# Optimization experiments

Hardware: AMD Instinct MI355X
Metric: run time of the kernel (lower is better)

The kernel has to match this reference:

```python
import jax, jax.numpy as jnp
import numpy as np

N = 16384   # total nodes
M = 512     # molecules
D_IN = 64
D_OUT = 64
NEG = -1e9  # mask value for nodes outside a molecule


def setup_inputs() -> dict:
    key = jax.random.key(0)
    ks = jax.random.split(key, 8)
    node_features = jax.random.normal(ks[0], (N, D_IN), dtype=jnp.float32)
    e = jax.random.uniform(ks[1], (N, N), dtype=jnp.float32) * (2.0 / N)
    # molecule membership: sorted segment ids -> one-hot membership matrix
    seg = np.sort(np.asarray(jax.random.randint(ks[2], (N,), 0, M)))
    mnm = (seg[None, :] == np.arange(M)[:, None]).astype(np.float32)
    mol_node_matrix = jnp.asarray(mnm)
    mol_node_mask = jnp.asarray((1.0 - mnm) * NEG)
    s = 1.0 / np.sqrt(D_IN)
    W0 = jax.random.uniform(ks[3], (D_OUT, D_IN), jnp.float32, -s, s)
    b0 = jnp.zeros((D_OUT,), jnp.float32)
    W1 = jax.random.uniform(ks[4], (D_OUT, D_OUT), jnp.float32, -s, s)
    b1 = jnp.zeros((D_OUT,), jnp.float32)
    w2 = jax.random.uniform(ks[5], (1, D_OUT), jnp.float32, -s, s)
    b2 = jnp.zeros((1,), jnp.float32)
    return dict(node_features=node_features, e=e,
                mol_node_matrix=mol_node_matrix, mol_node_mask=mol_node_mask,
                W0=W0, b0=b0, W1=W1, b1=b1, w2=w2, b2=b2)


def reference(node_features, e, mol_node_matrix, mol_node_mask, W0, b0, W1, b1, w2, b2):
    # GraphConvolutionLayer: two linears with adjacency matmul, LeakyReLU between
    h = e @ (node_features @ W0.T + b0)            # [N, D_OUT]
    h = jax.nn.leaky_relu(h, negative_slope=0.01)
    h = e @ (h @ W1.T + b1)                        # [N, D_OUT]
    h = jnp.tanh(h)
    # attention logits per node; mol_node_matrix @ diag(a) == mnm * a^T (broadcast)
    a = (h @ w2.T + b2).reshape(-1)                # [N]
    logits = mol_node_matrix * a[None, :] + mol_node_mask  # [M, N]
    mol_node_weight = jax.nn.softmax(logits, axis=1)
    return mol_node_weight @ h, mol_node_weight
```

## Files before the change

kernel.cpp:

```cpp
#include <hip/hip_runtime.h>
#include <hip/hip_bf16.h>

#define NN 16384
#define MM 512
#define DD 64
#define BK 128
#define BM 32
#define ITERS (NN / BK)
#define BK2 256
#define ITERS2 (NN / BK2)

typedef __attribute__((ext_vector_type(8))) short short8;
typedef __attribute__((ext_vector_type(4))) float f32x4;
typedef __attribute__((ext_vector_type(4))) short short4v;
typedef __attribute__((ext_vector_type(4))) unsigned u32x4;

#define SE 2097152.0f
#define INV_SE 4.76837158203125e-07f

__device__ __forceinline__ short f2bf(float f) {
  union { __hip_bfloat16 b; short s; } u;
  u.b = __float2bfloat16(f);
  return u.s;
}

__device__ __forceinline__ short8 cvt8(f32x4 a, f32x4 b) {
  short8 r;
  r[0] = f2bf(a[0]); r[1] = f2bf(a[1]); r[2] = f2bf(a[2]); r[3] = f2bf(a[3]);
  r[4] = f2bf(b[0]); r[5] = f2bf(b[1]); r[6] = f2bf(b[2]); r[7] = f2bf(b[3]);
  return r;
}

typedef __attribute__((address_space(1))) const unsigned gu32;
typedef __attribute__((address_space(3))) unsigned lu32;
__device__ __forceinline__ void gld16(const void* g, void* l) {
  __builtin_amdgcn_global_load_lds((gu32*)g, (lu32*)l, 16, 0, 0);
}

template <int OFMT>
__global__ __launch_bounds__(256) void linear_mfma(const float* __restrict__ in,
                                                   const float* __restrict__ W,
                                                   const float* __restrict__ b,
                                                   void* __restrict__ xt_) {
  const int t = threadIdx.x, lane = t & 63, w = t >> 6;
  const int rl = lane & 15, hi = lane >> 4;
  const int r0 = blockIdx.x * 64 + w * 16;
  const float* ap = in + (size_t)(r0 + rl) * DD + hi * 8;

  f32x4 acc[4];
#pragma unroll
  for (int g = 0; g < 4; ++g) {
    const float bias = b[g * 16 + rl];
    acc[g][0] = bias; acc[g][1] = bias; acc[g][2] = bias; acc[g][3] = bias;
  }
#pragma unroll
  for (int kk = 0; kk < DD; kk += 32) {
    const short8 af = cvt8(*(const f32x4*)(ap + kk), *(const f32x4*)(ap + kk + 4));
#pragma unroll
    for (int g = 0; g < 4; ++g) {
      const float* wp = W + (size_t)(g * 16 + rl) * DD + hi * 8 + kk;
      const short8 wf = cvt8(*(const f32x4*)wp, *(const f32x4*)(wp + 4));
      acc[g] = __builtin_amdgcn_mfma_f32_16x16x32_bf16(af, wf, acc[g], 0, 0, 0);
    }
  }
#pragma unroll
  for (int g = 0; g < 4; ++g) {
    if (OFMT == 0) {
      unsigned short* xt = (unsigned short*)xt_;
      short4v s;
      s[0] = f2bf(acc[g][0]); s[1] = f2bf(acc[g][1]);
      s[2] = f2bf(acc[g][2]); s[3] = f2bf(acc[g][3]);
      *(short4v*)(xt + (size_t)(g * 16 + rl) * NN + r0 + hi * 4) = s;
    } else {
      unsigned char* xt = (unsigned char*)xt_;
      int pk = __builtin_amdgcn_cvt_pk_fp8_f32(acc[g][0], acc[g][1], 0, false);
      pk = __builtin_amdgcn_cvt_pk_fp8_f32(acc[g][2], acc[g][3], pk, true);
      *(unsigned*)(xt + (size_t)(g * 16 + rl) * NN + r0 + hi * 4) = (unsigned)pk;
    }
  }
}

__global__ __launch_bounds__(256) void gemm1(const float* __restrict__ e,
                                             const unsigned short* __restrict__ xt,
                                             float* __restrict__ out,
                                             unsigned char* __restrict__ e8) {
  __shared__ float Ab[2][BM * BK];
  __shared__ unsigned short Bb[2][64 * BK];
  const int t = threadIdx.x, lane = t & 63, w = t >> 6;
  const int rl = lane & 15, hi = lane >> 4;
  const int wr = w >> 1, wc = w & 1;
  const int r0 = blockIdx.x * BM;
  const int it0 = (blockIdx.x * 37) & (ITERS - 1);

  auto STAGE = [&](int buf, int it) {
    const int k0 = ((it0 + it) & (ITERS - 1)) * BK;
#pragma unroll
    for (int j = 0; j < 4; ++j) {
      const int row = w * 8 + j * 2 + (lane >> 5);
      const float* src =
          e + (size_t)(r0 + row) * NN + k0 + (((lane & 31) ^ (row & 7)) << 2);
      gld16(src, &Ab[buf][(w * 8 + j * 2) * BK]);
    }
#pragma unroll
    for (int j = 0; j < 4; ++j) {
      const int col = w * 16 + j * 4 + (lane >> 4);
      const unsigned short* src =
          xt + (size_t)col * NN + k0 + (((lane & 15) ^ (col & 7)) << 3);
      gld16(src, &Bb[buf][(w * 16 + j * 4) * BK]);
    }
  };

  f32x4 acc[2];
  acc[0][0] = acc[0][1] = acc[0][2] = acc[0][3] = 0.f;
  acc[1][0] = acc[1][1] = acc[1][2] = acc[1][3] = 0.f;

  STAGE(0, 0);
#pragma unroll 1
  for (int it = 0; it < ITERS; ++it) {
    const int cur = it & 1;
    const int k0c = ((it0 + it) & (ITERS - 1)) * BK;
    if (it + 1 < ITERS) {
      STAGE(cur ^ 1, it + 1);
      asm volatile("s_waitcnt vmcnt(9)" ::: "memory");
    } else {
      asm volatile("s_waitcnt vmcnt(0)" ::: "memory");
    }
    __builtin_amdgcn_s_barrier();
    asm volatile("" ::: "memory");
#pragma unroll
    for (int kk = 0; kk < BK; kk += 32) {
      const int ca = (kk >> 2) + hi * 2;
      const int arow = (wr * 16 + rl) * BK;
      f32x4 a0 = *(const f32x4*)&Ab[cur][arow + ((ca ^ (rl & 7)) << 2)];
      f32x4 a1 = *(const f32x4*)&Ab[cur][arow + (((ca + 1) ^ (rl & 7)) << 2)];
      const short8 af = cvt8(a0, a1);
      const int cb = (kk >> 3) + hi;
#pragma unroll
      for (int g = 0; g < 2; ++g) {
        const int col = wc * 32 + g * 16 + rl;
        const short8 bf =
            *(const short8*)&Bb[cur][col * BK + ((cb ^ (rl & 7)) << 3)];
        acc[g] = __builtin_amdgcn_mfma_f32_16x16x32_bf16(af, bf, acc[g], 0, 0, 0);
      }
    }
    {
      const int r = t >> 3, j0 = t & 7;
      const float* arow = &Ab[cur][r * BK];
      u32x4 dw;
#pragma unroll
      for (int i = 0; i < 4; ++i) {
        const int c = j0 * 4 + i;
        f32x4 q = *(const f32x4*)&arow[(c ^ (r & 7)) << 2];
        int d = __builtin_amdgcn_cvt_pk_fp8_f32(q[0] * SE, q[1] * SE, 0, false);
        d = __builtin_amdgcn_cvt_pk_fp8_f32(q[2] * SE, q[3] * SE, d, true);
        dw[i] = (unsigned)d;
      }
      *(u32x4*)(e8 + (size_t)(r0 + r) * NN + k0c + j0 * 16) = dw;
    }
    asm volatile("" ::: "memory");
    __builtin_amdgcn_s_barrier();
  }

#pragma unroll
  for (int g = 0; g < 2; ++g) {
    const int col = wc * 32 + g * 16 + rl;
#pragma unroll
    for (int j = 0; j < 4; ++j) {
      float v = acc[g][j];
      v = (v > 0.f) ? v : 0.01f * v;
      out[(size_t)(r0 + wr * 16 + hi * 4 + j) * DD + col] = v;
    }
  }
}

__global__ __launch_bounds__(256) void gemm2_fp8(const unsigned char* __restrict__ e8,
                                                 const unsigned char* __restrict__ xt8,
                                                 float* __restrict__ out) {
  __shared__ unsigned char Ab2[2][BM * BK2];
  __shared__ unsigned char Bb2[2][64 * BK2];
  const int t = threadIdx.x, lane = t & 63, w = t >> 6;
  const int rl = lane & 15, hi = lane >> 4;
  const int wr = w >> 1, wc = w & 1;
  const int r0 = blockIdx.x * BM;
  const int it0 = (blockIdx.x * 37) & (ITERS2 - 1);

  auto STAGE = [&](int buf, int it) {
    const int k0 = ((it0 + it) & (ITERS2 - 1)) * BK2;
#pragma unroll
    for (int j = 0; j < 2; ++j) {
      const int row = w * 8 + j * 4 + (lane >> 4);
      const unsigned char* src =
          e8 + (size_t)(r0 + row) * NN + k0 + (((lane & 15) ^ (row & 15)) << 4);
      gld16(src, &Ab2[buf][(w * 8 + j * 4) * BK2]);
    }
#pragma unroll
    for (int j = 0; j < 4; ++j) {
      const int col = w * 16 + j * 4 + (lane >> 4);
      const unsigned char* src =
          xt8 + (size_t)col * NN + k0 + (((lane & 15) ^ (col & 15)) << 4);
      gld16(src, &Bb2[buf][(w * 16 + j * 4) * BK2]);
    }
  };

  f32x4 acc[2];
  acc[0][0] = acc[0][1] = acc[0][2] = acc[0][3] = 0.f;
  acc[1][0] = acc[1][1] = acc[1][2] = acc[1][3] = 0.f;

  STAGE(0, 0);
#pragma unroll 1
  for (int it = 0; it < ITERS2; ++it) {
    const int cur = it & 1;
    if (it + 1 < ITERS2) {
      STAGE(cur ^ 1, it + 1);
      asm volatile("s_waitcnt vmcnt(6)" ::: "memory");
    } else {
      asm volatile("s_waitcnt vmcnt(0)" ::: "memory");
    }
    __builtin_amdgcn_s_barrier();
    asm volatile("" ::: "memory");
    const unsigned char* arow = &Ab2[cur][(wr * 16 + rl) * BK2];
#pragma unroll
    for (int kk = 0; kk < BK2; kk += 32) {
      const int ca = (kk >> 4) + (hi >> 1);
      const int off = (hi & 1) * 8;
      const long af = *(const long*)&arow[((ca ^ (rl & 15)) << 4) + off];
#pragma unroll
      for (int g = 0; g < 2; ++g) {
        const int col = wc * 32 + g * 16 + rl;
        const long bf =
            *(const long*)&Bb2[cur][col * BK2 + ((ca ^ (col & 15)) << 4) + off];
        acc[g] = __builtin_amdgcn_mfma_f32_16x16x32_fp8_fp8(af, bf, acc[g], 0, 0, 0);
      }
    }
    asm volatile("" ::: "memory");
    __builtin_amdgcn_s_barrier();
  }

#pragma unroll
  for (int g = 0; g < 2; ++g) {
    const int col = wc * 32 + g * 16 + rl;
#pragma unroll
    for (int j = 0; j < 4; ++j) {
      float v = tanhf(acc[g][j] * INV_SE);
      out[(size_t)(r0 + wr * 16 + hi * 4 + j) * DD + col] = v;
    }
  }
}

__global__ __launch_bounds__(256) void a_kernel(const float* __restrict__ h,
                                                const float* __restrict__ w2,
                                                const float* __restrict__ b2,
                                                float* __restrict__ a) {
  const int t = threadIdx.x;
  const int lane = t & 63;
  const int n = blockIdx.x * 4 + (t >> 6);
  float v = h[(size_t)n * DD + lane] * w2[lane];
#pragma unroll
  for (int off = 32; off > 0; off >>= 1) v += __shfl_xor(v, off);
  if (lane == 0) a[n] = v + b2[0];
}

__global__ __launch_bounds__(256) void softmax_kernel(const float* __restrict__ mnm,
                                                      const float* __restrict__ a,
                                                      float* __restrict__ wout) {
  __shared__ float red[256];
  const int m = blockIdx.x, t = threadIdx.x;
  const size_t base = (size_t)m * NN;
  const f32x4* mnm4 = (const f32x4*)(mnm + base);
  const f32x4* a4 = (const f32x4*)a;
  f32x4* wout4 = (f32x4*)(wout + base);

  f32x4 lg[16];
  float mx = -3.0e38f;
#pragma unroll
  for (int i = 0; i < 16; ++i) {
    const int idx = t + i * 256;
    const f32x4 mv = mnm4[idx];
    const f32x4 av = a4[idx];
    f32x4 v;
#pragma unroll
    for (int j = 0; j < 4; ++j) v[j] = (mv[j] > 0.5f) ? av[j] : -3.0e38f;
    lg[i] = v;
    mx = fmaxf(mx, fmaxf(fmaxf(v[0], v[1]), fmaxf(v[2], v[3])));
  }
  red[t] = mx; __syncthreads();
  for (int s = 128; s > 0; s >>= 1) {
    if (t < s) red[t] = fmaxf(red[t], red[t + s]);
    __syncthreads();
  }
  mx = red[0]; __syncthreads();
  const bool empty = (mx < -1.0e38f);
  float sm = 0.f;
#pragma unroll
  for (int i = 0; i < 16; ++i) {
    f32x4 v = lg[i];
#pragma unroll
    for (int j = 0; j < 4; ++j)
      v[j] = empty ? 1.0f : ((v[j] > -1.0e38f) ? expf(v[j] - mx) : 0.0f);
    lg[i] = v;
    sm += v[0] + v[1] + v[2] + v[3];
  }
  red[t] = sm; __syncthreads();
  for (int s = 128; s > 0; s >>= 1) {
    if (t < s) red[t] += red[t + s];
    __syncthreads();
  }
  const float inv = 1.0f / red[0];
#pragma unroll
  for (int i = 0; i < 16; ++i) wout4[t + i * 256] = lg[i] * inv;
}

__global__ __launch_bounds__(256) void pool_kernel(const float* __restrict__ wmat,
                                                   const float* __restrict__ h,
                                                   float* __restrict__ out0) {
  __shared__ float wl[256];
  __shared__ float partial[4][64];
  const int m = blockIdx.x;
  const int t = threadIdx.x;
  const int d = t & 63;
  const int sub = t >> 6;
  float acc = 0.f;
  for (int c0 = 0; c0 < NN; c0 += 256) {
    float wv = wmat[(size_t)m * NN + c0 + t];
    __syncthreads();
    wl[t] = wv;
    if (__syncthreads_or(wv > 0.f)) {
      const float* hp = h + (size_t)(c0 + sub * 64) * DD + d;
      const float* wp = wl + sub * 64;
#pragma unroll 8
      for (int i = 0; i < 64; ++i) acc += wp[i] * hp[(size_t)i * DD];
    }
  }
  __syncthreads();
  partial[sub][d] = acc;
  __syncthreads();
  if (t < 64)
    out0[m * DD + t] =
        partial[0][t] + partial[1][t] + partial[2][t] + partial[3][t];
}

extern "C" void kernel_launch(void* const* d_in, const int* in_sizes, int n_in,
                              void* d_out, int out_size, void* d_ws, size_t ws_size,
                              hipStream_t stream) {
  const float* nf  = (const float*)d_in[0];
  const float* e   = (const float*)d_in[1];
  const float* mnm = (const float*)d_in[2];
  const float* W0  = (const float*)d_in[4];
  const float* b0  = (const float*)d_in[5];
  const float* W1  = (const float*)d_in[6];
  const float* b1  = (const float*)d_in[7];
  const float* w2  = (const float*)d_in[8];
  const float* b2  = (const float*)d_in[9];

  char* ws = (char*)d_ws;
  unsigned short* XT0 = (unsigned short*)(ws);
  unsigned char*  XT8 = (unsigned char*)(ws + (size_t)2 * 1024 * 1024);
  float* h1 = (float*)(ws + (size_t)4 * 1024 * 1024);
  float* h  = (float*)(ws + (size_t)8 * 1024 * 1024);
  float* av = (float*)(ws + (size_t)12 * 1024 * 1024);
  unsigned char* e8 = (unsigned char*)(ws + (size_t)16 * 1024 * 1024);

  float* out0 = (float*)d_out;
  float* wout = out0 + (size_t)MM * DD;

  linear_mfma<0><<<256, 256, 0, stream>>>(nf, W0, b0, XT0);
  gemm1<<<512, 256, 0, stream>>>(e, XT0, h1, e8);
  linear_mfma<1><<<256, 256, 0, stream>>>(h1, W1, b1, XT8);
  gemm2_fp8<<<512, 256, 0, stream>>>(e8, XT8, h);
  a_kernel<<<4096, 256, 0, stream>>>(h, w2, b2, av);
  softmax_kernel<<<512, 256, 0, stream>>>(mnm, av, wout);
  pool_kernel<<<512, 256, 0, stream>>>(wout, h, out0);
}
```

Measured before the change: 416.7 us.

## Fuse softmax with pooling over contiguous node range; reorder fp8 store before MFMA

Merges the softmax and pooling kernels into one. Each block finds the min and max member node index of its molecule and pools only over that contiguous range, instead of scanning all 16384 nodes and skipping chunks with zero weight. In gemm1, the fp8 conversion and store of the e tile now runs before the MFMA loop, which may change how memory and compute overlap. Pooling over only the index range assumes molecule members are contiguous, which holds because segment ids are sorted, and it rereads the weights it just wrote from global memory.

```diff
diff --git a/kernel.cpp b/kernel.cpp
--- a/kernel.cpp
+++ b/kernel.cpp
@@ -127,22 +127,6 @@
     }
     __builtin_amdgcn_s_barrier();
     asm volatile("" ::: "memory");
-#pragma unroll
-    for (int kk = 0; kk < BK; kk += 32) {
-      const int ca = (kk >> 2) + hi * 2;
-      const int arow = (wr * 16 + rl) * BK;
-      f32x4 a0 = *(const f32x4*)&Ab[cur][arow + ((ca ^ (rl & 7)) << 2)];
-      f32x4 a1 = *(const f32x4*)&Ab[cur][arow + (((ca + 1) ^ (rl & 7)) << 2)];
-      const short8 af = cvt8(a0, a1);
-      const int cb = (kk >> 3) + hi;
-#pragma unroll
-      for (int g = 0; g < 2; ++g) {
-        const int col = wc * 32 + g * 16 + rl;
-        const short8 bf =
-            *(const short8*)&Bb[cur][col * BK + ((cb ^ (rl & 7)) << 3)];
-        acc[g] = __builtin_amdgcn_mfma_f32_16x16x32_bf16(af, bf, acc[g], 0, 0, 0);
-      }
-    }
     {
       const int r = t >> 3, j0 = t & 7;
       const float* arow = &Ab[cur][r * BK];
@@ -156,6 +140,22 @@
         dw[i] = (unsigned)d;
       }
       *(u32x4*)(e8 + (size_t)(r0 + r) * NN + k0c + j0 * 16) = dw;
+    }
+#pragma unroll
+    for (int kk = 0; kk < BK; kk += 32) {
+      const int ca = (kk >> 2) + hi * 2;
+      const int arow = (wr * 16 + rl) * BK;
+      f32x4 a0 = *(const f32x4*)&Ab[cur][arow + ((ca ^ (rl & 7)) << 2)];
+      f32x4 a1 = *(const f32x4*)&Ab[cur][arow + (((ca + 1) ^ (rl & 7)) << 2)];
+      const short8 af = cvt8(a0, a1);
+      const int cb = (kk >> 3) + hi;
+#pragma unroll
+      for (int g = 0; g < 2; ++g) {
+        const int col = wc * 32 + g * 16 + rl;
+        const short8 bf =
+            *(const short8*)&Bb[cur][col * BK + ((cb ^ (rl & 7)) << 3)];
+        acc[g] = __builtin_amdgcn_mfma_f32_16x16x32_bf16(af, bf, acc[g], 0, 0, 0);
+      }
     }
     asm volatile("" ::: "memory");
     __builtin_amdgcn_s_barrier();
@@ -260,10 +260,14 @@
   if (lane == 0) a[n] = v + b2[0];
 }
 
-__global__ __launch_bounds__(256) void softmax_kernel(const float* __restrict__ mnm,
-                                                      const float* __restrict__ a,
-                                                      float* __restrict__ wout) {
+__global__ __launch_bounds__(256) void softmax_pool(const float* __restrict__ mnm,
+                                                    const float* __restrict__ a,
+                                                    const float* __restrict__ h,
+                                                    float* __restrict__ wout,
+                                                    float* __restrict__ out0) {
   __shared__ float red[256];
+  __shared__ int redi[256];
+  __shared__ float partial[4][64];
   const int m = blockIdx.x, t = threadIdx.x;
   const size_t base = (size_t)m * NN;
   const f32x4* mnm4 = (const f32x4*)(mnm + base);
@@ -272,6 +276,7 @@
 
   f32x4 lg[16];
   float mx = -3.0e38f;
+  int mn_n = NN, mx_n = -1;
 #pragma unroll
   for (int i = 0; i < 16; ++i) {
     const int idx = t + i * 256;
@@ -279,17 +284,38 @@
     const f32x4 av = a4[idx];
     f32x4 v;
 #pragma unroll
-    for (int j = 0; j < 4; ++j) v[j] = (mv[j] > 0.5f) ? av[j] : -3.0e38f;
+    for (int j = 0; j < 4; ++j) {
+      const bool mem = mv[j] > 0.5f;
+      v[j] = mem ? av[j] : -3.0e38f;
+      if (mem) {
+        const int n = idx * 4 + j;
+        mn_n = min(mn_n, n);
+        mx_n = max(mx_n, n);
+      }
+    }
     lg[i] = v;
     mx = fmaxf(mx, fmaxf(fmaxf(v[0], v[1]), fmaxf(v[2], v[3])));
   }
-  red[t] = mx; __syncthreads();
+  red[t] = mx; redi[t] = mn_n; __syncthreads();
   for (int s = 128; s > 0; s >>= 1) {
-    if (t < s) red[t] = fmaxf(red[t], red[t + s]);
+    if (t < s) {
+      red[t] = fmaxf(red[t], red[t + s]);
+      redi[t] = min(redi[t], redi[t + s]);
+    }
     __syncthreads();
   }
-  mx = red[0]; __syncthreads();
-  const bool empty = (mx < -1.0e38f);
+  mx = red[0];
+  const int ns = redi[0];
+  __syncthreads();
+  redi[t] = mx_n; __syncthreads();
+  for (int s = 128; s > 0; s >>= 1) {
+    if (t < s) redi[t] = max(redi[t], redi[t + s]);
+    __syncthreads();
+  }
+  const int ne = redi[0];
+  __syncthreads();
+
+  const bool empty = (ne < 0);
   float sm = 0.f;
 #pragma unroll
   for (int i = 0; i < 16; ++i) {
@@ -308,31 +334,18 @@
   const float inv = 1.0f / red[0];
 #pragma unroll
   for (int i = 0; i < 16; ++i) wout4[t + i * 256] = lg[i] * inv;
-}
-
-__global__ __launch_bounds__(256) void pool_kernel(const float* __restrict__ wmat,
-                                                   const float* __restrict__ h,
-                                                   float* __restrict__ out0) {
-  __shared__ float wl[256];
-  __shared__ float partial[4][64];
-  const int m = blockIdx.x;
-  const int t = threadIdx.x;
-  const int d = t & 63;
-  const int sub = t >> 6;
-  float acc = 0.f;
-  for (int c0 = 0; c0 < NN; c0 += 256) {
-    float wv = wmat[(size_t)m * NN + c0 + t];
-    __syncthreads();
-    wl[t] = wv;
-    if (__syncthreads_or(wv > 0.f)) {
-      const float* hp = h + (size_t)(c0 + sub * 64) * DD + d;
-      const float* wp = wl + sub * 64;
-#pragma unroll 8
-      for (int i = 0; i < 64; ++i) acc += wp[i] * hp[(size_t)i * DD];
-    }
-  }
+
+  __threadfence_block();
   __syncthreads();
-  partial[sub][d] = acc;
+
+  const int s0 = empty ? 0 : ns;
+  const int e0 = empty ? NN : ne + 1;
+  const int d = t & 63, sub = t >> 6;
+  const float* wrow = wout + base;
+  float accp = 0.f;
+  for (int n = s0 + sub; n < e0; n += 4)
+    accp += wrow[n] * h[(size_t)n * DD + d];
+  partial[sub][d] = accp;
   __syncthreads();
   if (t < 64)
     out0[m * DD + t] =
@@ -368,6 +381,5 @@
   linear_mfma<1><<<256, 256, 0, stream>>>(h1, W1, b1, XT8);
   gemm2_fp8<<<512, 256, 0, stream>>>(e8, XT8, h);
   a_kernel<<<4096, 256, 0, stream>>>(h, w2, b2, av);
-  softmax_kernel<<<512, 256, 0, stream>>>(mnm, av, wout);
-  pool_kernel<<<512, 256, 0, stream>>>(wout, h, out0);
-}
+  softmax_pool<<<512, 256, 0, stream>>>(mnm, av, h, wout, out0);
+}
```

Result: faster. 383.9 us (-7.9%).
